# Kernel optimization log

Hardware: AMD Instinct MI355X
Metric: run time of the kernel (lower is better)

Reference implementation:

```python
import jax, jax.numpy as jnp
import numpy as np

GAMMA = 1.5
BN_EPS = 1e-5


def sparsemax(z):
    """Sparsemax along last axis (Martins & Astudillo, 2016)."""
    z = z - jnp.max(z, axis=-1, keepdims=True)
    z_sorted = -jnp.sort(-z, axis=-1)                      # descending sort
    z_cumsum = jnp.cumsum(z_sorted, axis=-1)
    k = jnp.arange(1, z.shape[-1] + 1, dtype=z.dtype)
    support = (z_sorted - (z_cumsum - 1.0) / k) > 0
    k_z = jnp.clip(jnp.sum(support, axis=-1, keepdims=True), 1, None).astype(z.dtype)
    idx = (k_z - 1.0).astype(jnp.int32)
    tau = (jnp.take_along_axis(z_cumsum, idx, axis=-1) - 1.0) / k_z
    return jnp.clip(z - tau, 0.0, None)


def setup_inputs() -> dict:
    key = jax.random.key(0)
    k1, k2 = jax.random.split(key)
    B, T, E, H = 32, 512, 512, 8
    x = jax.random.normal(k1, (B, T, E), dtype=jnp.float32)
    # torch Linear weight (out, in), kaiming-ish scale
    W = jax.random.normal(k2, (H, E, E), dtype=jnp.float32) / np.float32(np.sqrt(E))
    bn_weight = jnp.ones((H, E), dtype=jnp.float32)
    bn_bias = jnp.zeros((H, E), dtype=jnp.float32)
    return {"x": x, "W": W, "bn_weight": bn_weight, "bn_bias": bn_bias}


def reference(x, W, bn_weight, bn_bias):
    B, T, E = x.shape
    H = W.shape[0]
    gi = x.reshape(B * T, E)
    # all-head linear: y[n,o] = sum_i gi[n,i] * W[h,o,i]
    logits = jnp.einsum('ni,hoi->hno', gi, W)              # (H, B*T, E)
    # BatchNorm1d in training mode: batch stats over the B*T axis, biased var
    mean = jnp.mean(logits, axis=1, keepdims=True)
    var = jnp.var(logits, axis=1, keepdims=True)
    logits = (logits - mean) / jnp.sqrt(var + BN_EPS)
    logits = logits * bn_weight[:, None, :] + bn_bias[:, None, :]
    logits = logits.reshape(H, B, T, E)

    prior0 = jnp.ones((B, T, E), dtype=x.dtype)

    def step(prior, logits_h):
        mask_h = sparsemax(logits_h * prior)
        prior = prior * jnp.clip(GAMMA - mask_h, 0.0, None)
        return prior, mask_h

    _, masks = jax.lax.scan(step, prior0, logits)          # masks: (H, B, T, E)
    masked_xs = x[None, :, :, :] * masks                   # (H, B, T, E)
    return masked_xs, jnp.transpose(masks, (1, 0, 2, 3))   # (B, H, T, E)
```

## Files before the change

### kernel.cpp

```cpp
#include <hip/hip_runtime.h>
#include <stdint.h>

#define Hh 8
#define Bb 32
#define Tt 512
#define Ee 512
#define Nn 16384
#define GAMMA_ 1.5f
#define BN_EPS_ 1e-5f

typedef _Float16 f16x4 __attribute__((ext_vector_type(4)));
typedef _Float16 f16x8 __attribute__((ext_vector_type(8)));
typedef float    f32x4 __attribute__((ext_vector_type(4)));

__device__ __forceinline__ void async_ld16(void* lds, const void* g) {
    __builtin_amdgcn_global_load_lds(
        (const __attribute__((address_space(1))) void*)g,
        (__attribute__((address_space(3))) void*)lds, 16, 0, 0);
}

__device__ __forceinline__ float dpp_sum64(float v) {
    int t;
    t = __builtin_amdgcn_update_dpp(0, __float_as_int(v), 0x111, 0xf, 0xf, true);
    v += __int_as_float(t);
    t = __builtin_amdgcn_update_dpp(0, __float_as_int(v), 0x112, 0xf, 0xf, true);
    v += __int_as_float(t);
    t = __builtin_amdgcn_update_dpp(0, __float_as_int(v), 0x114, 0xf, 0xf, true);
    v += __int_as_float(t);
    t = __builtin_amdgcn_update_dpp(0, __float_as_int(v), 0x118, 0xf, 0xf, true);
    v += __int_as_float(t);
    t = __builtin_amdgcn_update_dpp(0, __float_as_int(v), 0x142, 0xf, 0xf, true);
    v += __int_as_float(t);
    t = __builtin_amdgcn_update_dpp(0, __float_as_int(v), 0x143, 0xf, 0xf, true);
    v += __int_as_float(t);
    return __int_as_float(__builtin_amdgcn_readlane(__float_as_int(v), 63));
}

__device__ __forceinline__ float dpp_max64(float v) {
    int t;
    t = __builtin_amdgcn_update_dpp(__float_as_int(v), __float_as_int(v), 0x111, 0xf, 0xf, false);
    v = fmaxf(v, __int_as_float(t));
    t = __builtin_amdgcn_update_dpp(__float_as_int(v), __float_as_int(v), 0x112, 0xf, 0xf, false);
    v = fmaxf(v, __int_as_float(t));
    t = __builtin_amdgcn_update_dpp(__float_as_int(v), __float_as_int(v), 0x114, 0xf, 0xf, false);
    v = fmaxf(v, __int_as_float(t));
    t = __builtin_amdgcn_update_dpp(__float_as_int(v), __float_as_int(v), 0x118, 0xf, 0xf, false);
    v = fmaxf(v, __int_as_float(t));
    t = __builtin_amdgcn_update_dpp(__float_as_int(v), __float_as_int(v), 0x142, 0xf, 0xf, false);
    v = fmaxf(v, __int_as_float(t));
    t = __builtin_amdgcn_update_dpp(__float_as_int(v), __float_as_int(v), 0x143, 0xf, 0xf, false);
    v = fmaxf(v, __int_as_float(t));
    return __int_as_float(__builtin_amdgcn_readlane(__float_as_int(v), 63));
}

__global__ __launch_bounds__(256) void cvt_kernel(const float* __restrict__ x,
                                                  const float* __restrict__ W,
                                                  _Float16* __restrict__ xh,
                                                  _Float16* __restrict__ wh) {
    const int NX = Bb * Tt * Ee;
    int i = (blockIdx.x * 256 + threadIdx.x) * 4;
    if (i < NX) {
        float4 v = *(const float4*)(x + i);
        f16x4 o = {(_Float16)v.x, (_Float16)v.y, (_Float16)v.z, (_Float16)v.w};
        *(f16x4*)(xh + i) = o;
    } else {
        int j = i - NX;
        float4 v = *(const float4*)(W + j);
        f16x4 o = {(_Float16)v.x, (_Float16)v.y, (_Float16)v.z, (_Float16)v.w};
        *(f16x4*)(wh + j) = o;
    }
}

__global__ __launch_bounds__(512, 2) void gemm_kernel(const _Float16* __restrict__ A,
                                                      const _Float16* __restrict__ Bm,
                                                      _Float16* __restrict__ C,
                                                      float* __restrict__ sums,
                                                      float* __restrict__ sumsq) {
    __shared__ alignas(16) _Float16 As[2][256 * 32];
    __shared__ alignas(16) _Float16 Bs[2][256 * 32];
    const int id  = blockIdx.x;
    const int h   = id >> 7;
    const int rem = id & 127;
    const int mb  = (rem >> 1) * 256;
    const int nb  = (rem & 1) * 256;

    const int t    = threadIdx.x;
    const int lane = t & 63;
    const int w    = t >> 6;
    const int wrow = (w >> 2) * 128;
    const int wcol = (w & 3) * 64;
    const int quad = lane >> 4;
    const int l16  = lane & 15;

    const int kc = ((t & 3) - ((t >> 3) & 3)) & 3;
    const _Float16* Ap = A + (size_t)(mb + (t >> 2)) * Ee + kc * 8;
    const _Float16* Bp = Bm + (size_t)h * Ee * Ee + (size_t)(nb + (t >> 2)) * Ee + kc * 8;

    f32x4 acc[8][4] = {};

    async_ld16(&As[0][t * 8],        Ap);
    async_ld16(&As[0][4096 + t * 8], Ap + 128 * Ee);
    async_ld16(&Bs[0][t * 8],        Bp);
    async_ld16(&Bs[0][4096 + t * 8], Bp + 128 * Ee);

    const int so = ((quad + (l16 >> 1)) & 3) * 8;

    int buf = 0;
    for (int k0 = 0; k0 < Ee; k0 += 32) {
        __syncthreads();
        if (k0 + 32 < Ee) {
            int nx = buf ^ 1;
            async_ld16(&As[nx][t * 8],        Ap + k0 + 32);
            async_ld16(&As[nx][4096 + t * 8], Ap + 128 * Ee + k0 + 32);
            async_ld16(&Bs[nx][t * 8],        Bp + k0 + 32);
            async_ld16(&Bs[nx][4096 + t * 8], Bp + 128 * Ee + k0 + 32);
        }
        f16x8 b8[4];
#pragma unroll
        for (int nt = 0; nt < 4; ++nt)
            b8[nt] = *(const f16x8*)(&Bs[buf][(wcol + nt * 16 + l16) * 32 + so]);
#pragma unroll
        for (int mt = 0; mt < 8; ++mt) {
            f16x8 a8 = *(const f16x8*)(&As[buf][(wrow + mt * 16 + l16) * 32 + so]);
#pragma unroll
            for (int nt = 0; nt < 4; ++nt)
                acc[mt][nt] = __builtin_amdgcn_mfma_f32_16x16x32_f16(a8, b8[nt], acc[mt][nt], 0, 0, 0);
        }
        buf ^= 1;
    }

#pragma unroll
    for (int nt = 0; nt < 4; ++nt) {
        float sv = 0.f, ss = 0.f;
#pragma unroll
        for (int mt = 0; mt < 8; ++mt)
#pragma unroll
            for (int rr = 0; rr < 4; ++rr) { float v = acc[mt][nt][rr]; sv += v; ss += v * v; }
        sv += __shfl_xor(sv, 16, 64); sv += __shfl_xor(sv, 32, 64);
        ss += __shfl_xor(ss, 16, 64); ss += __shfl_xor(ss, 32, 64);
        if (quad == 0) {
            int col = nb + wcol + nt * 16 + l16;
            atomicAdd(&sums[h * Ee + col], sv);
            atomicAdd(&sumsq[h * Ee + col], ss);
        }
    }

    _Float16* Cp = C + (size_t)h * Nn * Ee;
#pragma unroll
    for (int mt = 0; mt < 8; ++mt)
#pragma unroll
        for (int rr = 0; rr < 4; ++rr) {
            int row = mb + wrow + mt * 16 + quad * 4 + rr;
            size_t off = (size_t)row * Ee + nb + wcol + l16;
#pragma unroll
            for (int nt = 0; nt < 4; ++nt)
                Cp[off + nt * 16] = (_Float16)acc[mt][nt][rr];
        }
}

__global__ __launch_bounds__(256) void stats_kernel(const float* __restrict__ sums,
                                                    const float* __restrict__ sumsq,
                                                    const float* __restrict__ bnw,
                                                    const float* __restrict__ bnb,
                                                    float* __restrict__ cA,
                                                    float* __restrict__ cB) {
    int i = blockIdx.x * 256 + threadIdx.x;
    float mean = sums[i] * (1.0f / Nn);
    float var  = sumsq[i] * (1.0f / Nn) - mean * mean;
    float inv  = rsqrtf(var + BN_EPS_);
    float a    = bnw[i] * inv;
    cA[i] = a;
    cB[i] = bnb[i] - mean * a;
}

__global__ __launch_bounds__(256) void rows_kernel(const float* __restrict__ x,
                                                   const _Float16* __restrict__ lg,
                                                   const float* __restrict__ cA,
                                                   const float* __restrict__ cB,
                                                   float* __restrict__ out) {
    const int n    = blockIdx.x * 4 + (threadIdx.x >> 6);
    const int lane = threadIdx.x & 63;
    const int e0   = lane * 4;
    const int bb   = n >> 9;
    const int tt   = n & 511;

    float xr[8], prior[8];
    {
        const float* xp = x + (size_t)n * Ee;
        float4 x0 = *(const float4*)(xp + e0);
        float4 x1 = *(const float4*)(xp + 256 + e0);
        xr[0]=x0.x; xr[1]=x0.y; xr[2]=x0.z; xr[3]=x0.w;
        xr[4]=x1.x; xr[5]=x1.y; xr[6]=x1.z; xr[7]=x1.w;
    }
#pragma unroll
    for (int j = 0; j < 8; ++j) prior[j] = 1.0f;

    float* omx = out;
    float* omk = out + (size_t)Hh * Nn * Ee;

    const _Float16* lrow = lg + (size_t)n * Ee;
    f16x4 l0 = *(const f16x4*)(lrow + e0);
    f16x4 l1 = *(const f16x4*)(lrow + 256 + e0);

#pragma unroll 1
    for (int h = 0; h < Hh; ++h) {
        f16x4 p0 = l0, p1 = l1;
        if (h + 1 < Hh) {
            const _Float16* lnx = lrow + (size_t)(h + 1) * Nn * Ee;
            p0 = *(const f16x4*)(lnx + e0);
            p1 = *(const f16x4*)(lnx + 256 + e0);
        }
        float z[8];
        {
            const float* ap = cA + h * Ee + e0;
            const float* bp = cB + h * Ee + e0;
            float4 a0 = *(const float4*)(ap);
            float4 b0 = *(const float4*)(bp);
            float4 a1 = *(const float4*)(ap + 256);
            float4 b1 = *(const float4*)(bp + 256);
            z[0] = ((float)l0[0] * a0.x + b0.x) * prior[0];
            z[1] = ((float)l0[1] * a0.y + b0.y) * prior[1];
            z[2] = ((float)l0[2] * a0.z + b0.z) * prior[2];
            z[3] = ((float)l0[3] * a0.w + b0.w) * prior[3];
            z[4] = ((float)l1[0] * a1.x + b1.x) * prior[4];
            z[5] = ((float)l1[1] * a1.y + b1.y) * prior[5];
            z[6] = ((float)l1[2] * a1.z + b1.z) * prior[6];
            z[7] = ((float)l1[3] * a1.w + b1.w) * prior[7];
        }

        float mx = z[0];
#pragma unroll
        for (int j = 1; j < 8; ++j) mx = fmaxf(mx, z[j]);
        float tau = dpp_max64(mx) - 1.0f;
        int cprev = -1;
#pragma unroll 1
        for (int it = 0; it < 64; ++it) {
            float s2 = 0.f;
            int cnt = 0;
#pragma unroll
            for (int j = 0; j < 8; ++j) {
                bool p = z[j] > tau;
                s2 += p ? z[j] : 0.0f;
                cnt += (int)__popcll(__ballot(p));
            }
            float S = dpp_sum64(s2);
            if (cnt == cprev) break;
            cprev = cnt;
            tau = (S - 1.0f) / (float)cnt;
        }

        size_t oxoff = ((size_t)h * Nn + n) * Ee + e0;
        size_t okoff = (((size_t)bb * Hh + h) * Tt + tt) * Ee + e0;
        f32x4 vx, vm;
#pragma unroll
        for (int j = 0; j < 4; ++j) {
            float m = fmaxf(z[j] - tau, 0.0f);
            prior[j] *= fmaxf(GAMMA_ - m, 0.0f);
            vm[j] = m; vx[j] = xr[j] * m;
        }
        __builtin_nontemporal_store(vx, (f32x4*)(omx + oxoff));
        __builtin_nontemporal_store(vm, (f32x4*)(omk + okoff));
#pragma unroll
        for (int j = 0; j < 4; ++j) {
            float m = fmaxf(z[4 + j] - tau, 0.0f);
            prior[4 + j] *= fmaxf(GAMMA_ - m, 0.0f);
            vm[j] = m; vx[j] = xr[4 + j] * m;
        }
        __builtin_nontemporal_store(vx, (f32x4*)(omx + oxoff + 256));
        __builtin_nontemporal_store(vm, (f32x4*)(omk + okoff + 256));
        l0 = p0; l1 = p1;
    }
}

extern "C" void kernel_launch(void* const* d_in, const int* in_sizes, int n_in,
                              void* d_out, int out_size, void* d_ws, size_t ws_size,
                              hipStream_t stream) {
    const float* x   = (const float*)d_in[0];
    const float* W   = (const float*)d_in[1];
    const float* bnw = (const float*)d_in[2];
    const float* bnb = (const float*)d_in[3];
    float* out = (float*)d_out;

    uint8_t* ws = (uint8_t*)d_ws;
    _Float16* xh = (_Float16*)(ws);
    _Float16* wh = (_Float16*)(ws + 16777216);
    _Float16* lg = (_Float16*)(ws + 20971520);
    float* sums  = (float*)(ws + 155189248);
    float* sumsq = (float*)(ws + 155205632);
    float* cA    = (float*)(ws + 155222016);
    float* cB    = (float*)(ws + 155238400);

    hipMemsetAsync(sums, 0, 2 * 4096 * sizeof(float), stream);

    cvt_kernel<<<10240, 256, 0, stream>>>(x, W, xh, wh);
    gemm_kernel<<<1024, 512, 0, stream>>>(xh, wh, lg, sums, sumsq);
    stats_kernel<<<16, 256, 0, stream>>>(sums, sumsq, bnw, bnb, cA, cB);
    rows_kernel<<<4096, 256, 0, stream>>>(x, lg, cA, cB, out);
}
```

Measured before the change: 648.6 us.

## Deepen GEMM LDS pipeline to four stages with explicit vmcnt waits

```diff
diff --git a/kernel.cpp b/kernel.cpp
--- a/kernel.cpp
+++ b/kernel.cpp
@@ -76,8 +76,8 @@
                                                       _Float16* __restrict__ C,
                                                       float* __restrict__ sums,
                                                       float* __restrict__ sumsq) {
-    __shared__ alignas(16) _Float16 As[2][256 * 32];
-    __shared__ alignas(16) _Float16 Bs[2][256 * 32];
+    __shared__ alignas(16) _Float16 As[4][256 * 32];
+    __shared__ alignas(16) _Float16 Bs[4][256 * 32];
     const int id  = blockIdx.x;
     const int h   = id >> 7;
     const int rem = id & 127;
@@ -98,35 +98,48 @@
 
     f32x4 acc[8][4] = {};
 
-    async_ld16(&As[0][t * 8],        Ap);
-    async_ld16(&As[0][4096 + t * 8], Ap + 128 * Ee);
-    async_ld16(&Bs[0][t * 8],        Bp);
-    async_ld16(&Bs[0][4096 + t * 8], Bp + 128 * Ee);
+#pragma unroll
+    for (int s = 0; s < 3; ++s) {
+        const _Float16* Aps = Ap + s * 32;
+        const _Float16* Bps = Bp + s * 32;
+        async_ld16(&As[s][t * 8],        Aps);
+        async_ld16(&As[s][4096 + t * 8], Aps + 128 * Ee);
+        async_ld16(&Bs[s][t * 8],        Bps);
+        async_ld16(&Bs[s][4096 + t * 8], Bps + 128 * Ee);
+    }
 
     const int so = ((quad + (l16 >> 1)) & 3) * 8;
 
-    int buf = 0;
-    for (int k0 = 0; k0 < Ee; k0 += 32) {
-        __syncthreads();
-        if (k0 + 32 < Ee) {
-            int nx = buf ^ 1;
-            async_ld16(&As[nx][t * 8],        Ap + k0 + 32);
-            async_ld16(&As[nx][4096 + t * 8], Ap + 128 * Ee + k0 + 32);
-            async_ld16(&Bs[nx][t * 8],        Bp + k0 + 32);
-            async_ld16(&Bs[nx][4096 + t * 8], Bp + 128 * Ee + k0 + 32);
-        }
+#pragma unroll 1
+    for (int s = 0; s < 16; ++s) {
+        if (s < 14)       asm volatile("s_waitcnt vmcnt(8)" ::: "memory");
+        else if (s == 14) asm volatile("s_waitcnt vmcnt(4)" ::: "memory");
+        else              asm volatile("s_waitcnt vmcnt(0)" ::: "memory");
+        __builtin_amdgcn_s_barrier();
+        asm volatile("" ::: "memory");
+
+        if (s + 3 < 16) {
+            const int b = (s + 3) & 3;
+            const _Float16* Aps = Ap + (s + 3) * 32;
+            const _Float16* Bps = Bp + (s + 3) * 32;
+            async_ld16(&As[b][t * 8],        Aps);
+            async_ld16(&As[b][4096 + t * 8], Aps + 128 * Ee);
+            async_ld16(&Bs[b][t * 8],        Bps);
+            async_ld16(&Bs[b][4096 + t * 8], Bps + 128 * Ee);
+        }
+
+        const int c = s & 3;
         f16x8 b8[4];
 #pragma unroll
         for (int nt = 0; nt < 4; ++nt)
-            b8[nt] = *(const f16x8*)(&Bs[buf][(wcol + nt * 16 + l16) * 32 + so]);
+            b8[nt] = *(const f16x8*)(&Bs[c][(wcol + nt * 16 + l16) * 32 + so]);
 #pragma unroll
         for (int mt = 0; mt < 8; ++mt) {
-            f16x8 a8 = *(const f16x8*)(&As[buf][(wrow + mt * 16 + l16) * 32 + so]);
+            f16x8 a8 = *(const f16x8*)(&As[c][(wrow + mt * 16 + l16) * 32 + so]);
 #pragma unroll
             for (int nt = 0; nt < 4; ++nt)
                 acc[mt][nt] = __builtin_amdgcn_mfma_f32_16x16x32_f16(a8, b8[nt], acc[mt][nt], 0, 0, 0);
         }
-        buf ^= 1;
     }
 
 #pragma unroll
```

Result: slower. 666.5 us (+2.8%).

## Deepen GEMM K-tile to 64 with XOR swizzle, block remap and MFMA priority

Applied to the files above, without the earlier changes.

```diff
diff --git a/kernel.cpp b/kernel.cpp
--- a/kernel.cpp
+++ b/kernel.cpp
@@ -76,9 +76,9 @@
                                                       _Float16* __restrict__ C,
                                                       float* __restrict__ sums,
                                                       float* __restrict__ sumsq) {
-    __shared__ alignas(16) _Float16 As[2][256 * 32];
-    __shared__ alignas(16) _Float16 Bs[2][256 * 32];
-    const int id  = blockIdx.x;
+    __shared__ alignas(16) _Float16 As[2][256 * 64];
+    __shared__ alignas(16) _Float16 Bs[2][256 * 64];
+    const int id  = (blockIdx.x & 7) * 128 + (blockIdx.x >> 3);
     const int h   = id >> 7;
     const int rem = id & 127;
     const int mb  = (rem >> 1) * 256;
@@ -92,41 +92,61 @@
     const int quad = lane >> 4;
     const int l16  = lane & 15;
 
-    const int kc = ((t & 3) - ((t >> 3) & 3)) & 3;
-    const _Float16* Ap = A + (size_t)(mb + (t >> 2)) * Ee + kc * 8;
-    const _Float16* Bp = Bm + (size_t)h * Ee * Ee + (size_t)(nb + (t >> 2)) * Ee + kc * 8;
+    const int c = ((t & 7) - ((t >> 4) & 7)) & 7;
+    const _Float16* Ap = A + (size_t)(mb + (t >> 3)) * Ee + c * 8;
+    const _Float16* Bp = Bm + (size_t)h * Ee * Ee + (size_t)(nb + (t >> 3)) * Ee + c * 8;
 
     f32x4 acc[8][4] = {};
 
-    async_ld16(&As[0][t * 8],        Ap);
-    async_ld16(&As[0][4096 + t * 8], Ap + 128 * Ee);
-    async_ld16(&Bs[0][t * 8],        Bp);
-    async_ld16(&Bs[0][4096 + t * 8], Bp + 128 * Ee);
-
-    const int so = ((quad + (l16 >> 1)) & 3) * 8;
-
-    int buf = 0;
-    for (int k0 = 0; k0 < Ee; k0 += 32) {
-        __syncthreads();
-        if (k0 + 32 < Ee) {
-            int nx = buf ^ 1;
-            async_ld16(&As[nx][t * 8],        Ap + k0 + 32);
-            async_ld16(&As[nx][4096 + t * 8], Ap + 128 * Ee + k0 + 32);
-            async_ld16(&Bs[nx][t * 8],        Bp + k0 + 32);
-            async_ld16(&Bs[nx][4096 + t * 8], Bp + 128 * Ee + k0 + 32);
-        }
-        f16x8 b8[4];
+#pragma unroll
+    for (int q = 0; q < 4; ++q) {
+        async_ld16(&As[0][q * 4096 + t * 8], Ap + q * 64 * Ee);
+        async_ld16(&Bs[0][q * 4096 + t * 8], Bp + q * 64 * Ee);
+    }
+
+#pragma unroll 1
+    for (int tile = 0; tile < 8; ++tile) {
+        const int cur = tile & 1;
+        asm volatile("s_waitcnt vmcnt(0)" ::: "memory");
+        __builtin_amdgcn_s_barrier();
+        asm volatile("" ::: "memory");
+
+        if (tile < 7) {
+            const _Float16* Aps = Ap + (tile + 1) * 64;
+            const _Float16* Bps = Bp + (tile + 1) * 64;
+#pragma unroll
+            for (int q = 0; q < 4; ++q) {
+                async_ld16(&As[cur ^ 1][q * 4096 + t * 8], Aps + q * 64 * Ee);
+                async_ld16(&Bs[cur ^ 1][q * 4096 + t * 8], Bps + q * 64 * Ee);
+            }
+        }
+
+        f16x8 b8[4][2];
 #pragma unroll
         for (int nt = 0; nt < 4; ++nt)
-            b8[nt] = *(const f16x8*)(&Bs[buf][(wcol + nt * 16 + l16) * 32 + so]);
+#pragma unroll
+            for (int kk = 0; kk < 2; ++kk) {
+                int row  = wcol + nt * 16 + l16;
+                int slot = ((kk * 4 + quad) + ((row >> 1) & 7)) & 7;
+                b8[nt][kk] = *(const f16x8*)(&Bs[cur][row * 64 + slot * 8]);
+            }
 #pragma unroll
         for (int mt = 0; mt < 8; ++mt) {
-            f16x8 a8 = *(const f16x8*)(&As[buf][(wrow + mt * 16 + l16) * 32 + so]);
-#pragma unroll
-            for (int nt = 0; nt < 4; ++nt)
-                acc[mt][nt] = __builtin_amdgcn_mfma_f32_16x16x32_f16(a8, b8[nt], acc[mt][nt], 0, 0, 0);
-        }
-        buf ^= 1;
+            f16x8 a8[2];
+#pragma unroll
+            for (int kk = 0; kk < 2; ++kk) {
+                int row  = wrow + mt * 16 + l16;
+                int slot = ((kk * 4 + quad) + ((row >> 1) & 7)) & 7;
+                a8[kk] = *(const f16x8*)(&As[cur][row * 64 + slot * 8]);
+            }
+            __builtin_amdgcn_s_setprio(1);
+#pragma unroll
+            for (int nt = 0; nt < 4; ++nt) {
+                acc[mt][nt] = __builtin_amdgcn_mfma_f32_16x16x32_f16(a8[0], b8[nt][0], acc[mt][nt], 0, 0, 0);
+                acc[mt][nt] = __builtin_amdgcn_mfma_f32_16x16x32_f16(a8[1], b8[nt][1], acc[mt][nt], 0, 0, 0);
+            }
+            __builtin_amdgcn_s_setprio(0);
+        }
     }
 
 #pragma unroll
```

Result: no change. 653.7 us (+0.8%).

## Triple-buffer GEMM LDS with split-phase ping-pong scheduling and block swizzle

Applied to the files above, without the earlier changes.

```diff
diff --git a/kernel.cpp b/kernel.cpp
--- a/kernel.cpp
+++ b/kernel.cpp
@@ -76,9 +76,9 @@
                                                       _Float16* __restrict__ C,
                                                       float* __restrict__ sums,
                                                       float* __restrict__ sumsq) {
-    __shared__ alignas(16) _Float16 As[2][256 * 32];
-    __shared__ alignas(16) _Float16 Bs[2][256 * 32];
-    const int id  = blockIdx.x;
+    __shared__ alignas(16) _Float16 As[3][256 * 32];
+    __shared__ alignas(16) _Float16 Bs[3][256 * 32];
+    const int id  = (blockIdx.x & 7) * 128 + (blockIdx.x >> 3);
     const int h   = id >> 7;
     const int rem = id & 127;
     const int mb  = (rem >> 1) * 256;
@@ -98,35 +98,68 @@
 
     f32x4 acc[8][4] = {};
 
-    async_ld16(&As[0][t * 8],        Ap);
-    async_ld16(&As[0][4096 + t * 8], Ap + 128 * Ee);
-    async_ld16(&Bs[0][t * 8],        Bp);
-    async_ld16(&Bs[0][4096 + t * 8], Bp + 128 * Ee);
+#pragma unroll
+    for (int s = 0; s < 2; ++s) {
+        async_ld16(&As[s][t * 8],        Ap + s * 32);
+        async_ld16(&As[s][4096 + t * 8], Ap + 128 * Ee + s * 32);
+        async_ld16(&Bs[s][t * 8],        Bp + s * 32);
+        async_ld16(&Bs[s][4096 + t * 8], Bp + 128 * Ee + s * 32);
+    }
 
     const int so = ((quad + (l16 >> 1)) & 3) * 8;
 
-    int buf = 0;
-    for (int k0 = 0; k0 < Ee; k0 += 32) {
-        __syncthreads();
-        if (k0 + 32 < Ee) {
-            int nx = buf ^ 1;
-            async_ld16(&As[nx][t * 8],        Ap + k0 + 32);
-            async_ld16(&As[nx][4096 + t * 8], Ap + 128 * Ee + k0 + 32);
-            async_ld16(&Bs[nx][t * 8],        Bp + k0 + 32);
-            async_ld16(&Bs[nx][4096 + t * 8], Bp + 128 * Ee + k0 + 32);
-        }
-        f16x8 b8[4];
+#pragma unroll 1
+    for (int tile = 0; tile < 16; ++tile) {
+        const int cur = tile % 3;
+        if (tile < 15) asm volatile("s_waitcnt vmcnt(4)" ::: "memory");
+        else           asm volatile("s_waitcnt vmcnt(0)" ::: "memory");
+        __builtin_amdgcn_s_barrier();
+        asm volatile("" ::: "memory");
+
+        const bool doStage = (tile + 2) < 16;
+        const int  nxt = (tile + 2) % 3;
+        const _Float16* Aps = Ap + (tile + 2) * 32;
+        const _Float16* Bps = Bp + (tile + 2) * 32;
+
+        f16x8 b8[4], a8[4];
 #pragma unroll
         for (int nt = 0; nt < 4; ++nt)
-            b8[nt] = *(const f16x8*)(&Bs[buf][(wcol + nt * 16 + l16) * 32 + so]);
-#pragma unroll
-        for (int mt = 0; mt < 8; ++mt) {
-            f16x8 a8 = *(const f16x8*)(&As[buf][(wrow + mt * 16 + l16) * 32 + so]);
+            b8[nt] = *(const f16x8*)(&Bs[cur][(wcol + nt * 16 + l16) * 32 + so]);
+#pragma unroll
+        for (int mt = 0; mt < 4; ++mt)
+            a8[mt] = *(const f16x8*)(&As[cur][(wrow + mt * 16 + l16) * 32 + so]);
+        if (doStage) {
+            async_ld16(&As[nxt][t * 8],        Aps);
+            async_ld16(&As[nxt][4096 + t * 8], Aps + 128 * Ee);
+        }
+        __builtin_amdgcn_s_barrier();
+        asm volatile("" ::: "memory");
+        __builtin_amdgcn_s_setprio(1);
+#pragma unroll
+        for (int mt = 0; mt < 4; ++mt)
 #pragma unroll
             for (int nt = 0; nt < 4; ++nt)
-                acc[mt][nt] = __builtin_amdgcn_mfma_f32_16x16x32_f16(a8, b8[nt], acc[mt][nt], 0, 0, 0);
-        }
-        buf ^= 1;
+                acc[mt][nt] = __builtin_amdgcn_mfma_f32_16x16x32_f16(a8[mt], b8[nt], acc[mt][nt], 0, 0, 0);
+        __builtin_amdgcn_s_setprio(0);
+        __builtin_amdgcn_s_barrier();
+        asm volatile("" ::: "memory");
+
+#pragma unroll
+        for (int mt = 0; mt < 4; ++mt)
+            a8[mt] = *(const f16x8*)(&As[cur][(wrow + (mt + 4) * 16 + l16) * 32 + so]);
+        if (doStage) {
+            async_ld16(&Bs[nxt][t * 8],        Bps);
+            async_ld16(&Bs[nxt][4096 + t * 8], Bps + 128 * Ee);
+        }
+        __builtin_amdgcn_s_barrier();
+        asm volatile("" ::: "memory");
+        __builtin_amdgcn_s_setprio(1);
+#pragma unroll
+        for (int mt = 0; mt < 4; ++mt)
+#pragma unroll
+            for (int nt = 0; nt < 4; ++nt)
+                acc[mt + 4][nt] = __builtin_amdgcn_mfma_f32_16x16x32_f16(a8[mt], b8[nt], acc[mt + 4][nt], 0, 0, 0);
+        __builtin_amdgcn_s_setprio(0);
     }
 
 #pragma unroll
```

New measurement: 649.6 us. No clear change (+0.2%).
